# Kernel optimization log

Measured on AMD Instinct MI355X. Metric: run time of the kernel, lower is better.

## Reference

```python
import jax, jax.numpy as jnp
import numpy as np


def setup_inputs() -> dict:
    key = jax.random.key(0)
    ks = jax.random.split(key, 6)
    b, t, k, h = 8, 128, 128, 4
    q_x = jax.random.normal(ks[0], (b, t, k), dtype=jnp.float32)
    kv_x = jax.random.normal(ks[1], (b, t, t - 1, k), dtype=jnp.float32)
    s = 1.0 / np.sqrt(k).astype(np.float32)
    Wk = jax.random.normal(ks[2], (k, k), dtype=jnp.float32) * s  # tokeys.weight
    Wq = jax.random.normal(ks[3], (k, k), dtype=jnp.float32) * s  # toqueries.weight
    Wv = jax.random.normal(ks[4], ((1 + k) * h, 2 * k), dtype=jnp.float32) * (1.0 / np.sqrt(2 * k).astype(np.float32))  # tovalues.weight
    bv = jax.random.normal(ks[5], ((1 + k) * h,), dtype=jnp.float32) * 0.01  # tovalues.bias
    return dict(q_x=q_x, kv_x=kv_x, Wk=Wk, Wq=Wq, Wv=Wv, bv=bv)


def reference(q_x, kv_x, Wk, Wq, Wv, bv):
    # kv_x: (b, t, t-1, k); q_x: (b, t, k)
    b, t, m, k = kv_x.shape  # m == t - 1
    h = Wv.shape[0] // (k + 1)
    # torch Linear: y = x @ W.T
    keys = jnp.einsum('btmk,jk->btmj', kv_x, Wk)          # (b,t,m,k)
    queries = jnp.einsum('btk,jk->btj', q_x, Wq)          # (b,t,k)
    queries = jnp.broadcast_to(queries[:, :, None, :], (b, t, m, k))
    value_input = jnp.concatenate([keys, queries], axis=-1)  # (b,t,m,2k)
    vals = jnp.einsum('btmc,oc->btmo', value_input, Wv) + bv  # (b,t,m,(1+k)h)
    vals = vals.reshape(b, t, m, h, k + 1)
    score = vals[..., 0]        # (b,t,m,h)
    values = vals[..., 1:]      # (b,t,m,h,k)
    w = jax.nn.softmax(score, axis=2)  # softmax over the t-1 (pair) axis
    x = jnp.einsum('btmh,btmhk->bthk', w, values)  # weighted sum over pairs
    return x.reshape(b, t, h * k)
```

## Files before the change

### kernel.cpp

```cpp
#include <hip/hip_runtime.h>

#define KD 128
#define NH 4
#define MM 127
#define NPRE 516

#define OFF_WC 0
#define OFF_C  131072

__global__ __launch_bounds__(256, 4)
void attn_fused(const float* __restrict__ kv_x,
                const float* __restrict__ Wk,
                const float* __restrict__ Wq,
                const float* __restrict__ Wv,
                float* __restrict__ ws) {
    const int bid = blockIdx.x;
    const int tid = threadIdx.x;

    if (bid < NPRE) {
        int o = bid;
        int h = o / 129, r = o - h * 129;
        if (r == 0) return;
        int dd = r - 1;
        int which = tid >> 7, k = tid & 127;
        const float* W = which ? Wq : Wk;
        const float* wvrow = Wv + (size_t)o * 256 + which * 128;
        float acc = 0.f;
        #pragma unroll 8
        for (int j = 0; j < 128; ++j)
            acc += wvrow[j] * W[j * 128 + k];
        ws[OFF_WC + (size_t)(h * 256 + which * 128 + k) * 128 + dd] = acc;
        return;
    }

    __shared__ float sW1s[NH * KD];
    __shared__ float ssc[512];
    __shared__ float swt[512];
    __shared__ float cpart[8][512];

    const int bt = bid - NPRE;
    const int dq = tid & 31;
    const int g  = tid >> 5;

    const float4* src = (const float4*)(kv_x + (size_t)bt * MM * KD);
    float4 kvr[16];
    #pragma unroll
    for (int k = 0; k < 16; ++k) {
        int idx = tid + k * 256;
        kvr[k] = (idx < MM * 32) ? src[idx] : make_float4(0.f, 0.f, 0.f, 0.f);
    }

    {
        int h0 = tid >> 7;
        int k  = tid & 127;
        const float* wv0 = Wv + (size_t)(129 * h0) * 256;
        const float* wv2 = Wv + (size_t)(129 * (h0 + 2)) * 256;
        float a0 = 0.f, a1 = 0.f;
        #pragma unroll 8
        for (int j = 0; j < 128; ++j) {
            float wk = Wk[j * 128 + k];
            a0 += wv0[j] * wk;
            a1 += wv2[j] * wk;
        }
        sW1s[h0 * 128 + k]       = a0;
        sW1s[(h0 + 2) * 128 + k] = a1;
    }
    __syncthreads();

    float4 w1s[NH];
    #pragma unroll
    for (int h = 0; h < NH; ++h)
        w1s[h] = *(const float4*)&sW1s[h * KD + dq * 4];

    const int bit4 = (tid >> 4) & 1;
    const int bit3 = (tid >> 3) & 1;
    const int myh  = bit4 * 2 + bit3;
    #pragma unroll
    for (int k = 0; k < 16; ++k) {
        float4 kv4 = kvr[k];
        float p0 = kv4.x*w1s[0].x + kv4.y*w1s[0].y + kv4.z*w1s[0].z + kv4.w*w1s[0].w;
        float p1 = kv4.x*w1s[1].x + kv4.y*w1s[1].y + kv4.z*w1s[1].z + kv4.w*w1s[1].w;
        float p2 = kv4.x*w1s[2].x + kv4.y*w1s[2].y + kv4.z*w1s[2].z + kv4.w*w1s[2].w;
        float p3 = kv4.x*w1s[3].x + kv4.y*w1s[3].y + kv4.z*w1s[3].z + kv4.w*w1s[3].w;
        float x = bit4 ? p0 : p2;
        float y = bit4 ? p1 : p3;
        float a = (bit4 ? p2 : p0) + __shfl_xor(x, 16);
        float b = (bit4 ? p3 : p1) + __shfl_xor(y, 16);
        float z = bit3 ? a : b;
        float v = (bit3 ? b : a) + __shfl_xor(z, 8);
        v += __shfl_xor(v, 4);
        v += __shfl_xor(v, 2);
        v += __shfl_xor(v, 1);
        int m = g + 8 * k;
        if ((tid & 7) == 0 && m < MM) ssc[m * 4 + myh] = v;
    }
    __syncthreads();

    {
        int h = tid >> 6, lane = tid & 63;
        float v0 = ssc[lane * 4 + h];
        bool has1 = (lane + 64) < MM;
        float v1 = has1 ? ssc[(lane + 64) * 4 + h] : -1e30f;
        float mx = fmaxf(v0, v1);
        #pragma unroll
        for (int off = 32; off; off >>= 1) mx = fmaxf(mx, __shfl_xor(mx, off));
        float e0 = __expf(v0 - mx);
        float e1 = has1 ? __expf(v1 - mx) : 0.f;
        float s = e0 + e1;
        #pragma unroll
        for (int off = 32; off; off >>= 1) s += __shfl_xor(s, off);
        float inv = 1.f / s;
        swt[lane * 4 + h] = e0 * inv;
        swt[(lane + 64) * 4 + h] = has1 ? e1 * inv : 0.f;
    }
    __syncthreads();

    float4 cacc[NH];
    #pragma unroll
    for (int h = 0; h < NH; ++h) cacc[h] = make_float4(0.f, 0.f, 0.f, 0.f);
    #pragma unroll
    for (int k = 0; k < 16; ++k) {
        int m = g + 8 * k;
        float4 wv  = *(const float4*)&swt[m * 4];
        float4 kv4 = kvr[k];
        cacc[0].x += wv.x*kv4.x; cacc[0].y += wv.x*kv4.y; cacc[0].z += wv.x*kv4.z; cacc[0].w += wv.x*kv4.w;
        cacc[1].x += wv.y*kv4.x; cacc[1].y += wv.y*kv4.y; cacc[1].z += wv.y*kv4.z; cacc[1].w += wv.y*kv4.w;
        cacc[2].x += wv.z*kv4.x; cacc[2].y += wv.z*kv4.y; cacc[2].z += wv.z*kv4.z; cacc[2].w += wv.z*kv4.w;
        cacc[3].x += wv.w*kv4.x; cacc[3].y += wv.w*kv4.y; cacc[3].z += wv.w*kv4.z; cacc[3].w += wv.w*kv4.w;
    }
    #pragma unroll
    for (int h = 0; h < NH; ++h)
        *(float4*)&cpart[g][h * KD + dq * 4] = cacc[h];
    __syncthreads();

    float* cdst = ws + OFF_C + (size_t)bt * 512;
    #pragma unroll
    for (int rep = 0; rep < 2; ++rep) {
        int o = tid + rep * 256;
        float s = 0.f;
        #pragma unroll
        for (int gg = 0; gg < 8; ++gg) s += cpart[gg][o];
        cdst[o] = s;
    }
}

#define BM 32
#define BN 64
#define BK 64
#define AP 34
#define BP 68

__global__ __launch_bounds__(256, 2)
void proj_out(const float* __restrict__ q_x,
              const float* __restrict__ bv,
              const float* __restrict__ ws,
              float* __restrict__ out) {
    __shared__ float sAT[BK][AP];
    __shared__ float sB[BK][BP];

    const int r0  = blockIdx.x * BM;
    const int dd0 = blockIdx.y * BN;
    const int h   = blockIdx.z;
    const int tid = threadIdx.x;
    const int tx  = tid & 15;
    const int ty  = tid >> 4;
    const float* cmat = ws + OFF_C;
    const float* Wct  = ws + OFF_WC;

    float acc[2][4];
    #pragma unroll
    for (int i = 0; i < 2; ++i)
        #pragma unroll
        for (int j = 0; j < 4; ++j) acc[i][j] = 0.f;

    for (int ks = 0; ks < 4; ++ks) {
        int kk0 = ks * BK;
        const float* Abase; int Astride;
        if (kk0 < 128) { Abase = cmat + h * KD + kk0; Astride = 512; }
        else           { Abase = q_x + (kk0 - 128);   Astride = KD;  }
        #pragma unroll
        for (int i = 0; i < 2; ++i) {
            int idx = tid + i * 256;
            int r = idx >> 4, c4 = idx & 15;
            float4 v = *(const float4*)(Abase + (size_t)(r0 + r) * Astride + c4 * 4);
            sAT[c4 * 4 + 0][r] = v.x;
            sAT[c4 * 4 + 1][r] = v.y;
            sAT[c4 * 4 + 2][r] = v.z;
            sAT[c4 * 4 + 3][r] = v.w;
        }
        #pragma unroll
        for (int i = 0; i < 4; ++i) {
            int idx = tid + i * 256;
            int c = idx >> 4, d4 = idx & 15;
            *(float4*)&sB[c][d4 * 4] =
                *(const float4*)(Wct + (size_t)(h * 256 + kk0 + c) * 128 + dd0 + d4 * 4);
        }
        __syncthreads();
        #pragma unroll 8
        for (int c = 0; c < BK; ++c) {
            float2 a  = *(const float2*)&sAT[c][ty * 2];
            float4 b4 = *(const float4*)&sB[c][tx * 4];
            acc[0][0] += a.x * b4.x; acc[0][1] += a.x * b4.y;
            acc[0][2] += a.x * b4.z; acc[0][3] += a.x * b4.w;
            acc[1][0] += a.y * b4.x; acc[1][1] += a.y * b4.y;
            acc[1][2] += a.y * b4.z; acc[1][3] += a.y * b4.w;
        }
        __syncthreads();
    }
    float bb[4];
    #pragma unroll
    for (int j = 0; j < 4; ++j) bb[j] = bv[h * 129 + 1 + dd0 + tx * 4 + j];
    #pragma unroll
    for (int i = 0; i < 2; ++i) {
        float4 v;
        v.x = acc[i][0] + bb[0];
        v.y = acc[i][1] + bb[1];
        v.z = acc[i][2] + bb[2];
        v.w = acc[i][3] + bb[3];
        *(float4*)(out + (size_t)(r0 + ty * 2 + i) * 512 + h * KD + dd0 + tx * 4) = v;
    }
}

extern "C" void kernel_launch(void* const* d_in, const int* in_sizes, int n_in,
                              void* d_out, int out_size, void* d_ws, size_t ws_size,
                              hipStream_t stream) {
    const float* q_x  = (const float*)d_in[0];
    const float* kv_x = (const float*)d_in[1];
    const float* Wk   = (const float*)d_in[2];
    const float* Wq   = (const float*)d_in[3];
    const float* Wv   = (const float*)d_in[4];
    const float* bv   = (const float*)d_in[5];
    float* out = (float*)d_out;
    float* ws  = (float*)d_ws;

    int bt = in_sizes[0] / KD;

    hipLaunchKernelGGL(attn_fused, dim3(NPRE + bt), dim3(256), 0, stream,
                       kv_x, Wk, Wq, Wv, ws);
    hipLaunchKernelGGL(proj_out, dim3(bt / BM, KD / BN, NH), dim3(256), 0, stream,
                       q_x, bv, ws, out);
}
```

Baseline: 45.56 us.

## Stage kv tile into LDS via direct global-to-LDS loads instead of registers

The per-(b,t) kv tile (127x128 floats, 64KB) is now loaded straight into shared memory with global_load_lds instead of into 16 float4 registers per thread. The load is issued after the W1s precompute, so it no longer overlaps with that work. The weighted-sum phase is restructured so only 128 threads each accumulate 32 rows, with a 4-way instead of 8-way partial reduction. The intent is to free register pressure; in exchange the kernel uses about 72KB of LDS per block, launch bounds drop to 2 blocks per SM, and half the threads sit idle in the accumulation phase.

```diff
diff --git a/kernel.cpp b/kernel.cpp
--- a/kernel.cpp
+++ b/kernel.cpp
@@ -8,7 +8,10 @@
 #define OFF_WC 0
 #define OFF_C  131072
 
-__global__ __launch_bounds__(256, 4)
+typedef const __attribute__((address_space(1))) void* gas_t;
+typedef __attribute__((address_space(3))) void* las_t;
+
+__global__ __launch_bounds__(256, 2)
 void attn_fused(const float* __restrict__ kv_x,
                 const float* __restrict__ Wk,
                 const float* __restrict__ Wq,
@@ -33,38 +36,43 @@
         return;
     }
 
+    __shared__ float skv[128 * KD];
     __shared__ float sW1s[NH * KD];
     __shared__ float ssc[512];
     __shared__ float swt[512];
-    __shared__ float cpart[8][512];
+    __shared__ float cpart[4][512];
 
     const int bt = bid - NPRE;
     const int dq = tid & 31;
     const int g  = tid >> 5;
-
-    const float4* src = (const float4*)(kv_x + (size_t)bt * MM * KD);
-    float4 kvr[16];
-    #pragma unroll
-    for (int k = 0; k < 16; ++k) {
-        int idx = tid + k * 256;
-        kvr[k] = (idx < MM * 32) ? src[idx] : make_float4(0.f, 0.f, 0.f, 0.f);
-    }
+    const int wv_ = tid >> 6;
 
     {
         int h0 = tid >> 7;
         int k  = tid & 127;
-        const float* wv0 = Wv + (size_t)(129 * h0) * 256;
-        const float* wv2 = Wv + (size_t)(129 * (h0 + 2)) * 256;
+        const float* r0 = Wv + (size_t)(129 * h0) * 256;
+        const float* r2 = Wv + (size_t)(129 * (h0 + 2)) * 256;
         float a0 = 0.f, a1 = 0.f;
         #pragma unroll 8
         for (int j = 0; j < 128; ++j) {
             float wk = Wk[j * 128 + k];
-            a0 += wv0[j] * wk;
-            a1 += wv2[j] * wk;
+            a0 += r0[j] * wk;
+            a1 += r2[j] * wk;
         }
         sW1s[h0 * 128 + k]       = a0;
         sW1s[(h0 + 2) * 128 + k] = a1;
     }
+
+    const float4* src = (const float4*)(kv_x + (size_t)bt * MM * KD);
+    #pragma unroll
+    for (int k = 0; k < 16; ++k) {
+        int idx  = tid + k * 256;
+        int gidx = (idx < MM * 32) ? idx : (MM * 32 - 1);
+        __builtin_amdgcn_global_load_lds((gas_t)(src + gidx),
+                                         (las_t)(&skv[(k * 256 + wv_ * 64) * 4]),
+                                         16, 0, 0);
+    }
+    asm volatile("s_waitcnt vmcnt(0)" ::: "memory");
     __syncthreads();
 
     float4 w1s[NH];
@@ -77,22 +85,22 @@
     const int myh  = bit4 * 2 + bit3;
     #pragma unroll
     for (int k = 0; k < 16; ++k) {
-        float4 kv4 = kvr[k];
-        float p0 = kv4.x*w1s[0].x + kv4.y*w1s[0].y + kv4.z*w1s[0].z + kv4.w*w1s[0].w;
-        float p1 = kv4.x*w1s[1].x + kv4.y*w1s[1].y + kv4.z*w1s[1].z + kv4.w*w1s[1].w;
-        float p2 = kv4.x*w1s[2].x + kv4.y*w1s[2].y + kv4.z*w1s[2].z + kv4.w*w1s[2].w;
-        float p3 = kv4.x*w1s[3].x + kv4.y*w1s[3].y + kv4.z*w1s[3].z + kv4.w*w1s[3].w;
+        int m = g + 8 * k;
+        float4 v = *(const float4*)&skv[m * KD + dq * 4];
+        float p0 = v.x*w1s[0].x + v.y*w1s[0].y + v.z*w1s[0].z + v.w*w1s[0].w;
+        float p1 = v.x*w1s[1].x + v.y*w1s[1].y + v.z*w1s[1].z + v.w*w1s[1].w;
+        float p2 = v.x*w1s[2].x + v.y*w1s[2].y + v.z*w1s[2].z + v.w*w1s[2].w;
+        float p3 = v.x*w1s[3].x + v.y*w1s[3].y + v.z*w1s[3].z + v.w*w1s[3].w;
         float x = bit4 ? p0 : p2;
         float y = bit4 ? p1 : p3;
         float a = (bit4 ? p2 : p0) + __shfl_xor(x, 16);
         float b = (bit4 ? p3 : p1) + __shfl_xor(y, 16);
         float z = bit3 ? a : b;
-        float v = (bit3 ? b : a) + __shfl_xor(z, 8);
-        v += __shfl_xor(v, 4);
-        v += __shfl_xor(v, 2);
-        v += __shfl_xor(v, 1);
-        int m = g + 8 * k;
-        if ((tid & 7) == 0 && m < MM) ssc[m * 4 + myh] = v;
+        float vr = (bit3 ? b : a) + __shfl_xor(z, 8);
+        vr += __shfl_xor(vr, 4);
+        vr += __shfl_xor(vr, 2);
+        vr += __shfl_xor(vr, 1);
+        if ((tid & 7) == 0 && m < MM) ssc[m * 4 + myh] = vr;
     }
     __syncthreads();
 
@@ -115,32 +123,40 @@
     }
     __syncthreads();
 
-    float4 cacc[NH];
-    #pragma unroll
-    for (int h = 0; h < NH; ++h) cacc[h] = make_float4(0.f, 0.f, 0.f, 0.f);
-    #pragma unroll
-    for (int k = 0; k < 16; ++k) {
-        int m = g + 8 * k;
-        float4 wv  = *(const float4*)&swt[m * 4];
-        float4 kv4 = kvr[k];
-        cacc[0].x += wv.x*kv4.x; cacc[0].y += wv.x*kv4.y; cacc[0].z += wv.x*kv4.z; cacc[0].w += wv.x*kv4.w;
-        cacc[1].x += wv.y*kv4.x; cacc[1].y += wv.y*kv4.y; cacc[1].z += wv.y*kv4.z; cacc[1].w += wv.y*kv4.w;
-        cacc[2].x += wv.z*kv4.x; cacc[2].y += wv.z*kv4.y; cacc[2].z += wv.z*kv4.z; cacc[2].w += wv.z*kv4.w;
-        cacc[3].x += wv.w*kv4.x; cacc[3].y += wv.w*kv4.y; cacc[3].z += wv.w*kv4.z; cacc[3].w += wv.w*kv4.w;
-    }
-    #pragma unroll
-    for (int h = 0; h < NH; ++h)
-        *(float4*)&cpart[g][h * KD + dq * 4] = cacc[h];
-    __syncthreads();
-
-    float* cdst = ws + OFF_C + (size_t)bt * 512;
-    #pragma unroll
-    for (int rep = 0; rep < 2; ++rep) {
-        int o = tid + rep * 256;
-        float s = 0.f;
-        #pragma unroll
-        for (int gg = 0; gg < 8; ++gg) s += cpart[gg][o];
-        cdst[o] = s;
+    if (tid < 128) {
+        const int cg = tid >> 5;
+        float4 ca0 = make_float4(0.f,0.f,0.f,0.f);
+        float4 ca1 = make_float4(0.f,0.f,0.f,0.f);
+        float4 ca2 = make_float4(0.f,0.f,0.f,0.f);
+        float4 ca3 = make_float4(0.f,0.f,0.f,0.f);
+        #pragma unroll 8
+        for (int r = 0; r < 32; ++r) {
+            int m = cg * 32 + r;
+            float4 w4 = *(const float4*)&swt[m * 4];
+            float4 kq = *(const float4*)&skv[m * KD + dq * 4];
+            ca0.x += w4.x*kq.x; ca0.y += w4.x*kq.y; ca0.z += w4.x*kq.z; ca0.w += w4.x*kq.w;
+            ca1.x += w4.y*kq.x; ca1.y += w4.y*kq.y; ca1.z += w4.y*kq.z; ca1.w += w4.y*kq.w;
+            ca2.x += w4.z*kq.x; ca2.y += w4.z*kq.y; ca2.z += w4.z*kq.z; ca2.w += w4.z*kq.w;
+            ca3.x += w4.w*kq.x; ca3.y += w4.w*kq.y; ca3.z += w4.w*kq.z; ca3.w += w4.w*kq.w;
+        }
+        *(float4*)&cpart[cg][0 * KD + dq * 4] = ca0;
+        *(float4*)&cpart[cg][1 * KD + dq * 4] = ca1;
+        *(float4*)&cpart[cg][2 * KD + dq * 4] = ca2;
+        *(float4*)&cpart[cg][3 * KD + dq * 4] = ca3;
+    }
+    __syncthreads();
+
+    if (tid < 128) {
+        float4 a = *(const float4*)&cpart[0][tid * 4];
+        float4 b = *(const float4*)&cpart[1][tid * 4];
+        float4 c = *(const float4*)&cpart[2][tid * 4];
+        float4 d = *(const float4*)&cpart[3][tid * 4];
+        float4 s;
+        s.x = a.x + b.x + c.x + d.x;
+        s.y = a.y + b.y + c.y + d.y;
+        s.z = a.z + b.z + c.z + d.z;
+        s.w = a.w + b.w + c.w + d.w;
+        *(float4*)(ws + OFF_C + (size_t)bt * 512 + tid * 4) = s;
     }
 }
 
```

New measurement: 52.38 us. +15.0%, slower.
